# Kernel tuning notes

Hardware: AMD Instinct MI355X
Metric: run time of the kernel (lower is better)

The kernel has to match this reference:

```python
import jax, jax.numpy as jnp
import numpy as np

B, T, IN, H, OUT = 512, 2048, 16, 128, 8


def setup_inputs() -> dict:
    key = jax.random.key(0)
    ks = jax.random.split(key, 12)
    s = 0.05
    return {
        "x": jax.random.normal(ks[0], (B, T, IN), dtype=jnp.float32),
        "W_ih0": jax.random.normal(ks[1], (3 * H, IN), dtype=jnp.float32) * s,
        "W_hh0": jax.random.normal(ks[2], (3 * H, H), dtype=jnp.float32) * s,
        "b_ih0": jax.random.normal(ks[3], (3 * H,), dtype=jnp.float32) * s,
        "b_hh0": jax.random.normal(ks[4], (3 * H,), dtype=jnp.float32) * s,
        "W_ih1": jax.random.normal(ks[5], (3 * H, H), dtype=jnp.float32) * s,
        "W_hh1": jax.random.normal(ks[6], (3 * H, H), dtype=jnp.float32) * s,
        "b_ih1": jax.random.normal(ks[7], (3 * H,), dtype=jnp.float32) * s,
        "b_hh1": jax.random.normal(ks[8], (3 * H,), dtype=jnp.float32) * s,
        "W_out": jax.random.normal(ks[9], (OUT, H), dtype=jnp.float32) * s,
        "b_out": jax.random.normal(ks[10], (OUT,), dtype=jnp.float32) * s,
    }


def _gru_cell(xg, h, W_hh, b_hh):
    # xg: precomputed x @ W_ih.T + b_ih, shape [B, 3H]; PyTorch gate order r,z,n
    hg = h @ W_hh.T + b_hh
    xr, xz, xn = jnp.split(xg, 3, axis=-1)
    hr, hz, hn = jnp.split(hg, 3, axis=-1)
    r = jax.nn.sigmoid(xr + hr)
    z = jax.nn.sigmoid(xz + hz)
    n = jnp.tanh(xn + r * hn)
    return (1.0 - z) * n + z * h


def reference(x, W_ih0, W_hh0, b_ih0, b_hh0, W_ih1, W_hh1, b_ih1, b_hh1, W_out, b_out):
    # Precompute layer-0 input gates for all timesteps: [T, B, 3H]
    xg0 = jnp.einsum('bti,gi->tbg', x, W_ih0) + b_ih0

    def step(carry, xg_t):
        h0, h1 = carry
        h0 = _gru_cell(xg_t, h0, W_hh0, b_hh0)
        xg1 = h0 @ W_ih1.T + b_ih1
        h1 = _gru_cell(xg1, h1, W_hh1, b_hh1)
        return (h0, h1), h1

    h0 = jnp.zeros((x.shape[0], W_hh0.shape[1]), dtype=x.dtype)
    h1 = jnp.zeros((x.shape[0], W_hh1.shape[1]), dtype=x.dtype)
    _, h1_seq = jax.lax.scan(step, (h0, h1), xg0)  # [T, B, H]
    out = jnp.einsum('tbh,oh->bto', h1_seq, W_out) + b_out  # [B, T, OUT]
    return out
```

## Files before the change

kernel.cpp:

```cpp
#include <hip/hip_runtime.h>


typedef unsigned int  uint;
typedef unsigned short ushort;
typedef _Float16 v8h __attribute__((ext_vector_type(8)));
typedef float    v4f __attribute__((ext_vector_type(4)));
typedef uint     v2u __attribute__((ext_vector_type(2)));

#define Tq   2048
#define INq  16
#define Hq   128
#define OUTq 8

#define MFMA(a,b,c) __builtin_amdgcn_mfma_f32_16x16x32_f16((a),(b),(c),0,0,0)
#define BAR() do { asm volatile("s_waitcnt lgkmcnt(0)" ::: "memory"); \
                   __builtin_amdgcn_s_barrier(); \
                   asm volatile("" ::: "memory"); } while(0)

__device__ __forceinline__ float sigm(float x){
  return __builtin_amdgcn_rcpf(1.0f + __expf(-x));
}
__device__ __forceinline__ float tanh_f(float x){
  return 1.0f - 2.0f*__builtin_amdgcn_rcpf(__expf(2.0f*x) + 1.0f);
}
__device__ __forceinline__ uint packh2(float lo, float hi){
  _Float16 a=(_Float16)lo, b=(_Float16)hi;
  return (uint)__builtin_bit_cast(ushort,a) | ((uint)__builtin_bit_cast(ushort,b)<<16);
}

__global__ __launch_bounds__(512,2) void gru2_kernel(
    const float* __restrict__ x,
    const float* __restrict__ Wih0, const float* __restrict__ Whh0,
    const float* __restrict__ bih0, const float* __restrict__ bhh0,
    const float* __restrict__ Wih1, const float* __restrict__ Whh1,
    const float* __restrict__ bih1, const float* __restrict__ bhh1,
    const float* __restrict__ Wout, const float* __restrict__ bout,
    float* __restrict__ out)
{
  const int tid  = threadIdx.x;
  const int lane = tid & 63;
  const int w    = tid >> 6;
  const int wl   = w & 3;
  const bool isL0 = (w < 4);
  const int nb   = lane & 15;
  const int bg   = lane >> 4;
  const int b0   = blockIdx.x * 16;

  __shared__ __align__(16) _Float16 hA0[2][2048];
  __shared__ __align__(16) _Float16 hA1[2][2048];
  __shared__ __align__(16) float    bl[1024];
  for (int i=tid; i<2048; i+=512){ ((uint*)hA0)[i]=0u; ((uint*)hA1)[i]=0u; }
  for (int i=tid; i<1024; i+=512){
    const int k=i>>7, h=i&127; float v;
    if      (k==0) v = bih0[h]       + bhh0[h];
    else if (k==1) v = bih0[128+h]   + bhh0[128+h];
    else if (k==2) v = bih0[256+h];
    else if (k==3) v = bhh0[256+h];
    else if (k==4) v = bih1[h]       + bhh1[h];
    else if (k==5) v = bih1[128+h]   + bhh1[128+h];
    else if (k==6) v = bih1[256+h];
    else           v = bhh1[256+h];
    bl[i]=v;
  }

  const float* xrow = x + (size_t)(b0+nb)*Tq*INq;
  float4 xfa, xfb;
  if (isL0 && bg < 2){
    xfa = *(const float4*)(xrow + bg*8);
    xfb = *(const float4*)(xrow + bg*8 + 4);
  }

  v8h W1[2][3][4], W2[2][3][4], W3[4];
  #pragma unroll
  for (int ta=0; ta<2; ++ta){
    const int R = 32*wl + 16*ta + nb;
    #pragma unroll
    for (int g=0; g<3; ++g){
      const int r = g*Hq + R;
      #pragma unroll
      for (int ks=0; ks<4; ++ks){
        const float* p1 = isL0 ? &Whh0[r*Hq + ks*32 + bg*8]
                               : &Wih1[r*Hq + ks*32 + bg*8];
        v8h a;
        #pragma unroll
        for (int e=0;e<8;++e) a[e]=(_Float16)p1[e];
        W1[ta][g][ks]=a;
      }
      if (isL0){
        v8h vx;
        #pragma unroll
        for (int e=0;e<8;++e) vx[e]=(_Float16)0.f;
        if (bg < 2){
          const float* p = &Wih0[r*INq + bg*8];
          #pragma unroll
          for (int e=0;e<8;++e) vx[e]=(_Float16)p[e];
        }
        W2[ta][g][0]=vx;
      } else {
        #pragma unroll
        for (int ks=0; ks<4; ++ks){
          const float* p2 = &Whh1[r*Hq + ks*32 + bg*8];
          v8h c;
          #pragma unroll
          for (int e=0;e<8;++e) c[e]=(_Float16)p2[e];
          W2[ta][ks==0?g:g][ks]=c;
        }
      }
    }
  }
  if (w == 3){
    #pragma unroll
    for (int ks=0; ks<4; ++ks){
      v8h v;
      #pragma unroll
      for (int e=0;e<8;++e) v[e]=(_Float16)0.f;
      if (nb < OUTq){
        const float* p = &Wout[nb*Hq + ks*32 + bg*8];
        #pragma unroll
        for (int e=0;e<8;++e) v[e]=(_Float16)p[e];
      }
      W3[ks]=v;
    }
  }
  v4f bo4 = {0.f,0.f,0.f,0.f};
  if (bg < 2) bo4 = *(const v4f*)(bout + bg*4);
  const v4f zf = {0.f,0.f,0.f,0.f};

  float hs[2][4] = {{0,0,0,0},{0,0,0,0}};

  int rb[4];
  #pragma unroll
  for (int ks=0; ks<4; ++ks) rb[ks] = nb*128 + ((ks*4+bg) ^ nb)*8;
  const int wof0 = nb*128 + (((4*wl + 0 + (bg>>1)) ^ nb))*8 + (bg&1)*4;
  const int wof1 = nb*128 + (((4*wl + 2 + (bg>>1)) ^ nb))*8 + (bg&1)*4;

  __syncthreads();

  for (int t=0; t<=Tq; ++t){
    const int pb = (t+1)&1;
    const int cb = t&1;

    if (isL0){
      if (t < Tq){
        v8h ax;
        #pragma unroll
        for (int e=0;e<8;++e) ax[e]=(_Float16)0.f;
        if (bg < 2){
          ax[0]=(_Float16)xfa.x; ax[1]=(_Float16)xfa.y; ax[2]=(_Float16)xfa.z; ax[3]=(_Float16)xfa.w;
          ax[4]=(_Float16)xfb.x; ax[5]=(_Float16)xfb.y; ax[6]=(_Float16)xfb.z; ax[7]=(_Float16)xfb.w;
          int tn = t+1; if (tn > Tq-1) tn = Tq-1;
          xfa = *(const float4*)(xrow + tn*INq + bg*8);
          xfb = *(const float4*)(xrow + tn*INq + bg*8 + 4);
        }
        v8h a0k[4];
        #pragma unroll
        for (int ks=0; ks<4; ++ks) a0k[ks] = *(const v8h*)&hA0[pb][rb[ks]];
        #pragma unroll
        for (int ta=0; ta<2; ++ta){
          const int hb4 = 32*wl + 16*ta + bg*4;
          v4f aR  = *(const v4f*)&bl[0*128+hb4];
          v4f aZ  = *(const v4f*)&bl[1*128+hb4];
          v4f aNX = *(const v4f*)&bl[2*128+hb4];
          v4f aNH = *(const v4f*)&bl[3*128+hb4];
          aR  = MFMA(W2[ta][0][0], ax, aR);
          aZ  = MFMA(W2[ta][1][0], ax, aZ);
          aNX = MFMA(W2[ta][2][0], ax, aNX);
          #pragma unroll
          for (int ks=0; ks<4; ++ks){
            aR  = MFMA(W1[ta][0][ks], a0k[ks], aR);
            aZ  = MFMA(W1[ta][1][ks], a0k[ks], aZ);
            aNH = MFMA(W1[ta][2][ks], a0k[ks], aNH);
          }
          float hn[4];
          #pragma unroll
          for (int j=0;j<4;++j){
            float r = sigm(aR[j]);
            float z = sigm(aZ[j]);
            float n = tanh_f(aNX[j] + r*aNH[j]);
            float h = n + z*(hs[ta][j]-n);
            hs[ta][j]=h; hn[j]=h;
          }
          v2u pk; pk[0]=packh2(hn[0],hn[1]); pk[1]=packh2(hn[2],hn[3]);
          *(v2u*)&hA0[cb][ta ? wof1 : wof0] = pk;
        }
      }
      if (w == 3 && t >= 1){
        v4f oac = zf;
        #pragma unroll
        for (int ks=0; ks<4; ++ks){
          v8h a1 = *(const v8h*)&hA1[cb][rb[ks]];
          oac = MFMA(W3[ks], a1, oac);
        }
        if (t >= 2 && bg < 2){
          float4 o;
          o.x=oac[0]+bo4[0]; o.y=oac[1]+bo4[1]; o.z=oac[2]+bo4[2]; o.w=oac[3]+bo4[3];
          *(float4*)&out[((size_t)(b0+nb)*Tq + (t-2))*OUTq + bg*4] = o;
        }
      }
    } else if (t >= 1){
      v8h a0k[4];
      #pragma unroll
      for (int ks=0; ks<4; ++ks) a0k[ks] = *(const v8h*)&hA0[pb][rb[ks]];
      #pragma unroll
      for (int ta=0; ta<2; ++ta){
        const int hb4 = 32*wl + 16*ta + bg*4;
        v4f cR  = *(const v4f*)&bl[4*128+hb4];
        v4f cZ  = *(const v4f*)&bl[5*128+hb4];
        v4f cNX = *(const v4f*)&bl[6*128+hb4];
        v4f cNH = *(const v4f*)&bl[7*128+hb4];
        #pragma unroll
        for (int ks=0; ks<4; ++ks){
          v8h a1 = *(const v8h*)&hA1[cb][rb[ks]];
          cR  = MFMA(W1[ta][0][ks], a0k[ks], cR);
          cZ  = MFMA(W1[ta][1][ks], a0k[ks], cZ);
          cNX = MFMA(W1[ta][2][ks], a0k[ks], cNX);
          cR  = MFMA(W2[ta][0][ks], a1, cR);
          cZ  = MFMA(W2[ta][1][ks], a1, cZ);
          cNH = MFMA(W2[ta][2][ks], a1, cNH);
        }
        float hn[4];
        #pragma unroll
        for (int j=0;j<4;++j){
          float r = sigm(cR[j]);
          float z = sigm(cZ[j]);
          float n = tanh_f(cNX[j] + r*cNH[j]);
          float h = n + z*(hs[ta][j]-n);
          hs[ta][j]=h; hn[j]=h;
        }
        v2u pk; pk[0]=packh2(hn[0],hn[1]); pk[1]=packh2(hn[2],hn[3]);
        *(v2u*)&hA1[pb][ta ? wof1 : wof0] = pk;
      }
    }
    BAR();
  }

  if (w == 3){
    v4f oac = zf;
    #pragma unroll
    for (int ks=0; ks<4; ++ks){
      v8h a1 = *(const v8h*)&hA1[1][rb[ks]];
      oac = MFMA(W3[ks], a1, oac);
    }
    if (bg < 2){
      float4 o;
      o.x=oac[0]+bo4[0]; o.y=oac[1]+bo4[1]; o.z=oac[2]+bo4[2]; o.w=oac[3]+bo4[3];
      *(float4*)&out[((size_t)(b0+nb)*Tq + (Tq-1))*OUTq + bg*4] = o;
    }
  }
}

extern "C" void kernel_launch(void* const* d_in, const int* in_sizes, int n_in,
                              void* d_out, int out_size, void* d_ws, size_t ws_size,
                              hipStream_t stream) {
  const float* x    = (const float*)d_in[0];
  const float* Wih0 = (const float*)d_in[1];
  const float* Whh0 = (const float*)d_in[2];
  const float* bih0 = (const float*)d_in[3];
  const float* bhh0 = (const float*)d_in[4];
  const float* Wih1 = (const float*)d_in[5];
  const float* Whh1 = (const float*)d_in[6];
  const float* bih1 = (const float*)d_in[7];
  const float* bhh1 = (const float*)d_in[8];
  const float* Wout = (const float*)d_in[9];
  const float* bo   = (const float*)d_in[10];
  gru2_kernel<<<dim3(32), dim3(512), 0, stream>>>(
      x, Wih0, Whh0, bih0, bhh0, Wih1, Whh1, bih1, bhh1, Wout, bo,
      (float*)d_out);
}
```

Measured before the change: 3.488 ms.

## Replace per-step block barrier with LDS progress-counter spin sync and 4-deep ring

Drops the block-wide s_barrier that ran after every timestep. Each layer wave now publishes its step counter in LDS and spins on the counters of the waves it depends on. Hidden-state buffers grow to a 4-slot ring, so layer 0 can run up to three steps ahead of layer 1. The output projection moves to wave 7 with its weights held in LDS, freeing registers. This relies on LDS ordering of volatile stores and adds spin-polling overhead and a risk of subtle race bugs.

```diff
diff --git a/kernel.cpp b/kernel.cpp
--- a/kernel.cpp
+++ b/kernel.cpp
@@ -13,9 +13,6 @@
 #define OUTq 8
 
 #define MFMA(a,b,c) __builtin_amdgcn_mfma_f32_16x16x32_f16((a),(b),(c),0,0,0)
-#define BAR() do { asm volatile("s_waitcnt lgkmcnt(0)" ::: "memory"); \
-                   __builtin_amdgcn_s_barrier(); \
-                   asm volatile("" ::: "memory"); } while(0)
 
 __device__ __forceinline__ float sigm(float x){
   return __builtin_amdgcn_rcpf(1.0f + __expf(-x));
@@ -27,6 +24,22 @@
   _Float16 a=(_Float16)lo, b=(_Float16)hi;
   return (uint)__builtin_bit_cast(ushort,a) | ((uint)__builtin_bit_cast(ushort,b)<<16);
 }
+__device__ __forceinline__ void spin2(volatile int* pa, int ta,
+                                      volatile int* pb, int tb){
+  for(;;){
+    int m0 = min(min(pa[0],pa[1]),min(pa[2],pa[3]));
+    int m1 = min(min(pb[0],pb[1]),min(pb[2],pb[3]));
+    if (m0 >= ta && m1 >= tb) break;
+    __builtin_amdgcn_s_sleep(1);
+  }
+  __builtin_amdgcn_sched_barrier(0);
+}
+#define PUBLISH(arr, idx, val) do {                          \
+  asm volatile("s_waitcnt lgkmcnt(0)" ::: "memory");         \
+  __builtin_amdgcn_sched_barrier(0);                         \
+  ((volatile int*)(arr))[idx] = (val);                       \
+  __builtin_amdgcn_sched_barrier(0);                         \
+} while(0)
 
 __global__ __launch_bounds__(512,2) void gru2_kernel(
     const float* __restrict__ x,
@@ -46,10 +59,13 @@
   const int bg   = lane >> 4;
   const int b0   = blockIdx.x * 16;
 
-  __shared__ __align__(16) _Float16 hA0[2][2048];
-  __shared__ __align__(16) _Float16 hA1[2][2048];
+  __shared__ __align__(16) _Float16 hA0[4][2048];
+  __shared__ __align__(16) _Float16 hA1[4][2048];
   __shared__ __align__(16) float    bl[1024];
-  for (int i=tid; i<2048; i+=512){ ((uint*)hA0)[i]=0u; ((uint*)hA1)[i]=0u; }
+  __shared__ __align__(16) _Float16 w3l[2048];
+  __shared__ int prog0[4], prog1[4];
+
+  for (int i=tid; i<4096; i+=512){ ((uint*)hA0)[i]=0u; ((uint*)hA1)[i]=0u; }
   for (int i=tid; i<1024; i+=512){
     const int k=i>>7, h=i&127; float v;
     if      (k==0) v = bih0[h]       + bhh0[h];
@@ -62,6 +78,7 @@
     else           v = bhh1[256+h];
     bl[i]=v;
   }
+  if (tid < 4){ prog0[tid]=0; prog1[tid]=0; }
 
   const float* xrow = x + (size_t)(b0+nb)*Tq*INq;
   float4 xfa, xfb;
@@ -70,7 +87,7 @@
     xfb = *(const float4*)(xrow + bg*8 + 4);
   }
 
-  v8h W1[2][3][4], W2[2][3][4], W3[4];
+  v8h W1[2][3][4], W2[2][3][4];
   #pragma unroll
   for (int ta=0; ta<2; ++ta){
     const int R = 32*wl + 16*ta + nb;
@@ -103,12 +120,12 @@
           v8h c;
           #pragma unroll
           for (int e=0;e<8;++e) c[e]=(_Float16)p2[e];
-          W2[ta][ks==0?g:g][ks]=c;
-        }
-      }
-    }
-  }
-  if (w == 3){
+          W2[ta][g][ks]=c;
+        }
+      }
+    }
+  }
+  if (w == 7){
     #pragma unroll
     for (int ks=0; ks<4; ++ks){
       v8h v;
@@ -119,7 +136,7 @@
         #pragma unroll
         for (int e=0;e<8;++e) v[e]=(_Float16)p[e];
       }
-      W3[ks]=v;
+      *(v8h*)&w3l[ks*512 + lane*8] = v;
     }
   }
   v4f bo4 = {0.f,0.f,0.f,0.f};
@@ -136,71 +153,60 @@
 
   __syncthreads();
 
-  for (int t=0; t<=Tq; ++t){
-    const int pb = (t+1)&1;
-    const int cb = t&1;
-
-    if (isL0){
-      if (t < Tq){
-        v8h ax;
-        #pragma unroll
-        for (int e=0;e<8;++e) ax[e]=(_Float16)0.f;
-        if (bg < 2){
-          ax[0]=(_Float16)xfa.x; ax[1]=(_Float16)xfa.y; ax[2]=(_Float16)xfa.z; ax[3]=(_Float16)xfa.w;
-          ax[4]=(_Float16)xfb.x; ax[5]=(_Float16)xfb.y; ax[6]=(_Float16)xfb.z; ax[7]=(_Float16)xfb.w;
-          int tn = t+1; if (tn > Tq-1) tn = Tq-1;
-          xfa = *(const float4*)(xrow + tn*INq + bg*8);
-          xfb = *(const float4*)(xrow + tn*INq + bg*8 + 4);
-        }
-        v8h a0k[4];
-        #pragma unroll
-        for (int ks=0; ks<4; ++ks) a0k[ks] = *(const v8h*)&hA0[pb][rb[ks]];
-        #pragma unroll
-        for (int ta=0; ta<2; ++ta){
-          const int hb4 = 32*wl + 16*ta + bg*4;
-          v4f aR  = *(const v4f*)&bl[0*128+hb4];
-          v4f aZ  = *(const v4f*)&bl[1*128+hb4];
-          v4f aNX = *(const v4f*)&bl[2*128+hb4];
-          v4f aNH = *(const v4f*)&bl[3*128+hb4];
-          aR  = MFMA(W2[ta][0][0], ax, aR);
-          aZ  = MFMA(W2[ta][1][0], ax, aZ);
-          aNX = MFMA(W2[ta][2][0], ax, aNX);
-          #pragma unroll
-          for (int ks=0; ks<4; ++ks){
-            aR  = MFMA(W1[ta][0][ks], a0k[ks], aR);
-            aZ  = MFMA(W1[ta][1][ks], a0k[ks], aZ);
-            aNH = MFMA(W1[ta][2][ks], a0k[ks], aNH);
-          }
-          float hn[4];
-          #pragma unroll
-          for (int j=0;j<4;++j){
-            float r = sigm(aR[j]);
-            float z = sigm(aZ[j]);
-            float n = tanh_f(aNX[j] + r*aNH[j]);
-            float h = n + z*(hs[ta][j]-n);
-            hs[ta][j]=h; hn[j]=h;
-          }
-          v2u pk; pk[0]=packh2(hn[0],hn[1]); pk[1]=packh2(hn[2],hn[3]);
-          *(v2u*)&hA0[cb][ta ? wof1 : wof0] = pk;
-        }
-      }
-      if (w == 3 && t >= 1){
-        v4f oac = zf;
-        #pragma unroll
-        for (int ks=0; ks<4; ++ks){
-          v8h a1 = *(const v8h*)&hA1[cb][rb[ks]];
-          oac = MFMA(W3[ks], a1, oac);
-        }
-        if (t >= 2 && bg < 2){
-          float4 o;
-          o.x=oac[0]+bo4[0]; o.y=oac[1]+bo4[1]; o.z=oac[2]+bo4[2]; o.w=oac[3]+bo4[3];
-          *(float4*)&out[((size_t)(b0+nb)*Tq + (t-2))*OUTq + bg*4] = o;
-        }
-      }
-    } else if (t >= 1){
+  if (isL0){
+    for (int t=0; t<Tq; ++t){
+      spin2(prog0, t, prog1, t-3);
+
+      v8h ax;
+      #pragma unroll
+      for (int e=0;e<8;++e) ax[e]=(_Float16)0.f;
+      if (bg < 2){
+        ax[0]=(_Float16)xfa.x; ax[1]=(_Float16)xfa.y; ax[2]=(_Float16)xfa.z; ax[3]=(_Float16)xfa.w;
+        ax[4]=(_Float16)xfb.x; ax[5]=(_Float16)xfb.y; ax[6]=(_Float16)xfb.z; ax[7]=(_Float16)xfb.w;
+        int tn = t+1; if (tn > Tq-1) tn = Tq-1;
+        xfa = *(const float4*)(xrow + tn*INq + bg*8);
+        xfb = *(const float4*)(xrow + tn*INq + bg*8 + 4);
+      }
       v8h a0k[4];
       #pragma unroll
-      for (int ks=0; ks<4; ++ks) a0k[ks] = *(const v8h*)&hA0[pb][rb[ks]];
+      for (int ks=0; ks<4; ++ks) a0k[ks] = *(const v8h*)&hA0[(t-1)&3][rb[ks]];
+      #pragma unroll
+      for (int ta=0; ta<2; ++ta){
+        const int hb4 = 32*wl + 16*ta + bg*4;
+        v4f aR  = *(const v4f*)&bl[0*128+hb4];
+        v4f aZ  = *(const v4f*)&bl[1*128+hb4];
+        v4f aNX = *(const v4f*)&bl[2*128+hb4];
+        v4f aNH = *(const v4f*)&bl[3*128+hb4];
+        aR  = MFMA(W2[ta][0][0], ax, aR);
+        aZ  = MFMA(W2[ta][1][0], ax, aZ);
+        aNX = MFMA(W2[ta][2][0], ax, aNX);
+        #pragma unroll
+        for (int ks=0; ks<4; ++ks){
+          aR  = MFMA(W1[ta][0][ks], a0k[ks], aR);
+          aZ  = MFMA(W1[ta][1][ks], a0k[ks], aZ);
+          aNH = MFMA(W1[ta][2][ks], a0k[ks], aNH);
+        }
+        float hn[4];
+        #pragma unroll
+        for (int j=0;j<4;++j){
+          float r = sigm(aR[j]);
+          float z = sigm(aZ[j]);
+          float n = tanh_f(aNX[j] + r*aNH[j]);
+          float h = n + z*(hs[ta][j]-n);
+          hs[ta][j]=h; hn[j]=h;
+        }
+        v2u pk; pk[0]=packh2(hn[0],hn[1]); pk[1]=packh2(hn[2],hn[3]);
+        *(v2u*)&hA0[t&3][ta ? wof1 : wof0] = pk;
+      }
+      PUBLISH(prog0, wl, t+1);
+    }
+  } else {
+    for (int t=0; t<Tq; ++t){
+      spin2(prog0, t+1, prog1, t);
+
+      v8h a0k[4];
+      #pragma unroll
+      for (int ks=0; ks<4; ++ks) a0k[ks] = *(const v8h*)&hA0[t&3][rb[ks]];
       #pragma unroll
       for (int ta=0; ta<2; ++ta){
         const int hb4 = 32*wl + 16*ta + bg*4;
@@ -210,7 +216,7 @@
         v4f cNH = *(const v4f*)&bl[7*128+hb4];
         #pragma unroll
         for (int ks=0; ks<4; ++ks){
-          v8h a1 = *(const v8h*)&hA1[cb][rb[ks]];
+          v8h a1 = *(const v8h*)&hA1[(t-1)&3][rb[ks]];
           cR  = MFMA(W1[ta][0][ks], a0k[ks], cR);
           cZ  = MFMA(W1[ta][1][ks], a0k[ks], cZ);
           cNX = MFMA(W1[ta][2][ks], a0k[ks], cNX);
@@ -228,23 +234,38 @@
           hs[ta][j]=h; hn[j]=h;
         }
         v2u pk; pk[0]=packh2(hn[0],hn[1]); pk[1]=packh2(hn[2],hn[3]);
-        *(v2u*)&hA1[pb][ta ? wof1 : wof0] = pk;
-      }
-    }
-    BAR();
-  }
-
-  if (w == 3){
-    v4f oac = zf;
-    #pragma unroll
-    for (int ks=0; ks<4; ++ks){
-      v8h a1 = *(const v8h*)&hA1[1][rb[ks]];
-      oac = MFMA(W3[ks], a1, oac);
-    }
-    if (bg < 2){
-      float4 o;
-      o.x=oac[0]+bo4[0]; o.y=oac[1]+bo4[1]; o.z=oac[2]+bo4[2]; o.w=oac[3]+bo4[3];
-      *(float4*)&out[((size_t)(b0+nb)*Tq + (Tq-1))*OUTq + bg*4] = o;
+        *(v2u*)&hA1[t&3][ta ? wof1 : wof0] = pk;
+      }
+      PUBLISH(prog1, wl, t+1);
+      if (w == 7 && t >= 1){
+        v4f oac = zf;
+        #pragma unroll
+        for (int ks=0; ks<4; ++ks){
+          v8h a1 = *(const v8h*)&hA1[(t-1)&3][rb[ks]];
+          v8h wf = *(const v8h*)&w3l[ks*512 + lane*8];
+          oac = MFMA(wf, a1, oac);
+        }
+        if (bg < 2){
+          float4 o;
+          o.x=oac[0]+bo4[0]; o.y=oac[1]+bo4[1]; o.z=oac[2]+bo4[2]; o.w=oac[3]+bo4[3];
+          *(float4*)&out[((size_t)(b0+nb)*Tq + (t-1))*OUTq + bg*4] = o;
+        }
+      }
+    }
+    if (w == 7){
+      spin2(prog1, Tq, prog1, Tq);
+      v4f oac = zf;
+      #pragma unroll
+      for (int ks=0; ks<4; ++ks){
+        v8h a1 = *(const v8h*)&hA1[(Tq-1)&3][rb[ks]];
+        v8h wf = *(const v8h*)&w3l[ks*512 + lane*8];
+        oac = MFMA(wf, a1, oac);
+      }
+      if (bg < 2){
+        float4 o;
+        o.x=oac[0]+bo4[0]; o.y=oac[1]+bo4[1]; o.z=oac[2]+bo4[2]; o.w=oac[3]+bo4[3];
+        *(float4*)&out[((size_t)(b0+nb)*Tq + (Tq-1))*OUTq + bg*4] = o;
+      }
     }
   }
 }
```

After: 3.644 ms. 1.04x slower.
